# Kernel optimization log

Measured on AMD Instinct MI355X. Metric: run time of the kernel, lower is better.

The kernel has to match this reference:

```python
import jax, jax.numpy as jnp
import numpy as np

HEADS = 8


def setup_inputs() -> dict:
    key = jax.random.key(0)
    ks = jax.random.split(key, 4)
    b, n, dim, inner = 8, 1024, 512, 512
    x = jax.random.normal(ks[0], (b, n, dim), jnp.float32)
    cp_mask = jax.random.randint(ks[1], (n, n), 0, 2, jnp.int32)  # binary core-periphery mask
    w_qkv = jax.random.normal(ks[2], (dim, 3 * inner), jnp.float32) * 0.02
    w_out = jax.random.normal(ks[3], (inner, dim), jnp.float32) * 0.02
    b_out = jnp.zeros((dim,), jnp.float32)
    return {"x": x, "cp_mask": cp_mask, "w_qkv": w_qkv, "w_out": w_out,
            "b_out": b_out, "patches_in_core_nodes": 16}


def reference(x, cp_mask, w_qkv, w_out, b_out, patches_in_core_nodes):
    b, n, dim = x.shape
    inner = w_qkv.shape[1] // 3
    dh = inner // HEADS
    scale = dh ** -0.5

    qkv = x @ w_qkv                                   # [b, n, 3*inner]
    q, k, v = jnp.split(qkv, 3, axis=-1)
    split_heads = lambda t: t.reshape(b, n, HEADS, dh).transpose(0, 2, 1, 3)
    q, k, v = map(split_heads, (q, k, v))             # [b, h, n, dh]

    mask = cp_mask.astype(x.dtype)                    # [n, n]
    dots_raw = jnp.einsum('bhnd,bhmd->bhnm', q, k)    # [b, h, n, n]

    # analysis pass: per-row mean |masked score|, summed over heads (detached in original)
    nnz = jnp.count_nonzero(cp_mask, axis=1).astype(x.dtype)       # [n]
    score = (jnp.abs(dots_raw * mask) * scale).sum(axis=1).sum(axis=-1) / nnz  # [b, n]
    score = jax.lax.stop_gradient(score)
    # original: list(np.argsort(score)) then list.reverse() -> batch order reversed
    idx = jnp.argsort(score, axis=-1)[::-1]           # [b, n]

    attn = jax.nn.softmax(dots_raw * scale * mask, axis=-1)
    out = jnp.einsum('bhnm,bhmd->bhnd', attn, v)      # [b, h, n, dh]
    out = out.transpose(0, 2, 1, 3).reshape(b, n, inner)

    # sequential row swap: out[j,i] <-> out[j,idx[j,i]] using the pristine clone
    out_clone = out
    bi = jnp.arange(b)
    for i in range(1, patches_in_core_nodes + 1):
        ti = idx[:, i]                                # [b]
        out = out.at[bi, i].set(out_clone[bi, ti])
        out = out.at[bi, ti].set(out_clone[:, i])
    return out @ w_out + b_out
```

## Files before the change

kernel.cpp:

```cpp
#include <hip/hip_runtime.h>
#include <hip/hip_bf16.h>

#define NN 1024
#define DH 64
#define DIM 512
#define INNER 512
#define QKV_N 1536
#define SCALE 0.125f
#define KPITCH 72
#define VPITCH 68
#define GPITCH 40

typedef short short8 __attribute__((ext_vector_type(8)));
typedef short short4v __attribute__((ext_vector_type(4)));
typedef float floatx4 __attribute__((ext_vector_type(4)));

static __device__ __forceinline__ unsigned short f2bf(float x) {
  __hip_bfloat16 h = __float2bfloat16(x);
  unsigned short u;
  __builtin_memcpy(&u, &h, 2);
  return u;
}
static __device__ __forceinline__ void splitbf(float x, unsigned short& hi, unsigned short& lo) {
  __hip_bfloat16 h = __float2bfloat16(x);
  float hf = __bfloat162float(h);
  __hip_bfloat16 l = __float2bfloat16(x - hf);
  __builtin_memcpy(&hi, &h, 2);
  __builtin_memcpy(&lo, &l, 2);
}

__global__ __launch_bounds__(64) void nnz_kernel(const int* __restrict__ mask,
                                                 float* __restrict__ nnzf,
                                                 unsigned long long* __restrict__ Mbits) {
  int row = blockIdx.x;
  int lane = threadIdx.x;
  const int* mrow = mask + (size_t)row * NN;
  int tot = 0;
  for (int mt = 0; mt < 16; ++mt) {
    unsigned long long bits = __ballot(mrow[mt * 64 + lane] != 0);
    if (lane == 0) {
      Mbits[(size_t)row * 16 + mt] = bits;
      tot += __popcll(bits);
    }
  }
  if (lane == 0) nnzf[row] = (float)tot;
}

__global__ __launch_bounds__(256) void split_kernel(const float* __restrict__ in,
                                                    unsigned short* __restrict__ hi,
                                                    unsigned short* __restrict__ lo,
                                                    int n4) {
  int i = blockIdx.x * 256 + threadIdx.x;
  if (i >= n4) return;
  float4 v = ((const float4*)in)[i];
  ushort4 h, l;
  splitbf(v.x, h.x, l.x);
  splitbf(v.y, h.y, l.y);
  splitbf(v.z, h.z, l.z);
  splitbf(v.w, h.w, l.w);
  ((ushort4*)hi)[i] = h;
  ((ushort4*)lo)[i] = l;
}

__global__ __launch_bounds__(256) void tsplit_kernel(const float* __restrict__ in, int K, int N,
                                                     unsigned short* __restrict__ hiT,
                                                     unsigned short* __restrict__ loT) {
  __shared__ float tile[32][33];
  int n0 = blockIdx.x * 32, k0 = blockIdx.y * 32;
  int t = threadIdx.x;
  int tn = t & 31, tk = t >> 5;
#pragma unroll
  for (int i = 0; i < 32; i += 8)
    tile[tk + i][tn] = in[(size_t)(k0 + tk + i) * N + n0 + tn];
  __syncthreads();
#pragma unroll
  for (int i = 0; i < 32; i += 8) {
    int n = tk + i;
    float v = tile[tn][n];
    unsigned short h, l;
    splitbf(v, h, l);
    hiT[(size_t)(n0 + n) * K + k0 + tn] = h;
    loT[(size_t)(n0 + n) * K + k0 + tn] = l;
  }
}

__global__ __launch_bounds__(256) void qkv_mfma(const unsigned short* __restrict__ xhi,
                                                const unsigned short* __restrict__ xlo,
                                                const unsigned short* __restrict__ bhiT,
                                                const unsigned short* __restrict__ bloT,
                                                unsigned short* __restrict__ qhi,
                                                unsigned short* __restrict__ qlo,
                                                unsigned short* __restrict__ khi,
                                                unsigned short* __restrict__ klo,
                                                unsigned short* __restrict__ vb) {
  __shared__ __align__(16) unsigned short Ah[128][GPITCH], Al[128][GPITCH];
  __shared__ __align__(16) unsigned short Bh[128][GPITCH], Bl[128][GPITCH];
  int t = threadIdx.x;
  int lane = t & 63, w = t >> 6;
  int wr = w >> 1, wc = w & 1;
  int s = lane & 15, q4 = lane >> 4;
  int r0 = blockIdx.y * 128, c0 = blockIdx.x * 128;

  floatx4 acc[4][4];
#pragma unroll
  for (int mi = 0; mi < 4; ++mi)
#pragma unroll
    for (int ni = 0; ni < 4; ++ni) { acc[mi][ni][0] = 0.f; acc[mi][ni][1] = 0.f; acc[mi][ni][2] = 0.f; acc[mi][ni][3] = 0.f; }

  for (int kt = 0; kt < DIM; kt += 32) {
    __syncthreads();
#pragma unroll
    for (int p = 0; p < 2; ++p) {
      int idx = p * 256 + t;
      int row = idx >> 2, kc = (idx & 3) * 8;
      *(short8*)&Ah[row][kc] = *(const short8*)&xhi[(size_t)(r0 + row) * DIM + kt + kc];
      *(short8*)&Al[row][kc] = *(const short8*)&xlo[(size_t)(r0 + row) * DIM + kt + kc];
      *(short8*)&Bh[row][kc] = *(const short8*)&bhiT[(size_t)(c0 + row) * DIM + kt + kc];
      *(short8*)&Bl[row][kc] = *(const short8*)&bloT[(size_t)(c0 + row) * DIM + kt + kc];
    }
    __syncthreads();
    short8 ah[4], al[4], bhf[4], blf[4];
#pragma unroll
    for (int mi = 0; mi < 4; ++mi) {
      ah[mi] = *(const short8*)&Ah[wr * 64 + mi * 16 + s][q4 * 8];
      al[mi] = *(const short8*)&Al[wr * 64 + mi * 16 + s][q4 * 8];
    }
#pragma unroll
    for (int ni = 0; ni < 4; ++ni) {
      bhf[ni] = *(const short8*)&Bh[wc * 64 + ni * 16 + s][q4 * 8];
      blf[ni] = *(const short8*)&Bl[wc * 64 + ni * 16 + s][q4 * 8];
    }
#pragma unroll
    for (int mi = 0; mi < 4; ++mi)
#pragma unroll
      for (int ni = 0; ni < 4; ++ni) {
        acc[mi][ni] = __builtin_amdgcn_mfma_f32_16x16x32_bf16(al[mi], bhf[ni], acc[mi][ni], 0, 0, 0);
        acc[mi][ni] = __builtin_amdgcn_mfma_f32_16x16x32_bf16(ah[mi], blf[ni], acc[mi][ni], 0, 0, 0);
        acc[mi][ni] = __builtin_amdgcn_mfma_f32_16x16x32_bf16(ah[mi], bhf[ni], acc[mi][ni], 0, 0, 0);
      }
  }

  int which = c0 >> 9;
#pragma unroll
  for (int mi = 0; mi < 4; ++mi)
#pragma unroll
    for (int ni = 0; ni < 4; ++ni) {
      int Cl = c0 + wc * 64 + ni * 16 + s;
      int cc = Cl & 511, h = cc >> 6, d = cc & 63;
#pragma unroll
      for (int i = 0; i < 4; ++i) {
        int R = r0 + wr * 64 + mi * 16 + q4 * 4 + i;
        int b = R >> 10, n = R & 1023;
        size_t o = (size_t)((((b << 3) + h) << 10) + n) * DH + d;
        float v = acc[mi][ni][i];
        if (which == 0) {
          unsigned short hh, ll;
          splitbf(SCALE * v, hh, ll);
          qhi[o] = hh; qlo[o] = ll;
        } else if (which == 1) {
          unsigned short hh, ll;
          splitbf(v, hh, ll);
          khi[o] = hh; klo[o] = ll;
        } else {
          vb[o] = f2bf(v);
        }
      }
    }
}

__global__ __launch_bounds__(256, 4) void attn_kernel(const unsigned short* __restrict__ qhi,
                                                      const unsigned short* __restrict__ qlo,
                                                      const unsigned short* __restrict__ khi,
                                                      const unsigned short* __restrict__ klo,
                                                      const unsigned short* __restrict__ vb,
                                                      const unsigned long long* __restrict__ Mbits,
                                                      unsigned short* __restrict__ ohi,
                                                      unsigned short* __restrict__ olo,
                                                      float* __restrict__ sph) {
  int bh = blockIdx.y;
  int rb = blockIdx.x;
  int b = bh >> 3, h = bh & 7;
  int row0 = rb * 64;
  int t = threadIdx.x;
  int lane = t & 63, w = t >> 6;
  int q4 = lane >> 4, s = lane & 15;
  int gr = 16 * w + s;

  __shared__ __align__(16) unsigned short Khs[64][KPITCH], Kls[64][KPITCH];
  __shared__ __align__(16) unsigned short Vts[64][VPITCH];
  __shared__ __align__(16) unsigned short Pss[64][KPITCH];
  __shared__ unsigned long long Mb[64];

  short8 aqh[2], aql[2];
  {
    size_t qb0 = ((size_t)bh * NN + row0 + gr) * DH;
#pragma unroll
    for (int ks = 0; ks < 2; ++ks) {
      aqh[ks] = *(const short8*)&qhi[qb0 + ks * 32 + q4 * 8];
      aql[ks] = *(const short8*)&qlo[qb0 + ks * 32 + q4 * 8];
    }
  }

  floatx4 Oacc[4];
  float Lacc[4], Sco[4];
#pragma unroll
  for (int j = 0; j < 4; ++j) { Oacc[j][0] = 0.f; Oacc[j][1] = 0.f; Oacc[j][2] = 0.f; Oacc[j][3] = 0.f; }
#pragma unroll
  for (int i = 0; i < 4; ++i) { Lacc[i] = 0.f; Sco[i] = 0.f; }

  for (int mt = 0; mt < 16; ++mt) {
    int m0 = mt * 64;
    __syncthreads();
#pragma unroll
    for (int p = 0; p < 2; ++p) {
      int idx = p * 256 + t;
      int n = idx >> 3, c8 = (idx & 7) * 8;
      size_t g = ((size_t)bh * NN + m0 + n) * DH + c8;
      *(short8*)&Khs[n][c8] = *(const short8*)&khi[g];
      *(short8*)&Kls[n][c8] = *(const short8*)&klo[g];
      short8 vv = *(const short8*)&vb[g];
#pragma unroll
      for (int j = 0; j < 8; ++j) Vts[c8 + j][n] = (unsigned short)vv[j];
    }
    if (t < 64) Mb[t] = Mbits[(size_t)(row0 + t) * 16 + mt];
    __syncthreads();

    floatx4 Sf[4];
#pragma unroll
    for (int j = 0; j < 4; ++j) { Sf[j][0] = 0.f; Sf[j][1] = 0.f; Sf[j][2] = 0.f; Sf[j][3] = 0.f; }
#pragma unroll
    for (int ks = 0; ks < 2; ++ks) {
      int d0 = ks * 32 + q4 * 8;
#pragma unroll
      for (int j = 0; j < 4; ++j) {
        short8 kh8 = *(const short8*)&Khs[16 * j + s][d0];
        short8 kl8 = *(const short8*)&Kls[16 * j + s][d0];
        Sf[j] = __builtin_amdgcn_mfma_f32_16x16x32_bf16(aql[ks], kh8, Sf[j], 0, 0, 0);
        Sf[j] = __builtin_amdgcn_mfma_f32_16x16x32_bf16(aqh[ks], kl8, Sf[j], 0, 0, 0);
        Sf[j] = __builtin_amdgcn_mfma_f32_16x16x32_bf16(aqh[ks], kh8, Sf[j], 0, 0, 0);
      }
    }

    unsigned long long mb[4];
#pragma unroll
    for (int i = 0; i < 4; ++i) mb[i] = Mb[16 * w + 4 * q4 + i];
    unsigned short pw[4][4];
#pragma unroll
    for (int j = 0; j < 4; ++j) {
#pragma unroll
      for (int i = 0; i < 4; ++i) {
        float sv = Sf[j][i];
        float mf = ((mb[i] >> (16 * j + s)) & 1ULL) ? 1.0f : 0.0f;
        Sco[i] += fabsf(sv) * mf;
        float p = __expf(sv * mf);
        Lacc[i] += p;
        pw[i][j] = f2bf(p);
      }
    }

#pragma unroll
    for (int i = 0; i < 4; ++i)
#pragma unroll
      for (int j = 0; j < 4; ++j) Pss[16 * w + 4 * q4 + i][16 * j + s] = pw[i][j];

#pragma unroll
    for (int ks = 0; ks < 2; ++ks) {
      int mm0 = ks * 32 + q4 * 8;
      short8 ap = *(const short8*)&Pss[gr][mm0];
#pragma unroll
      for (int j = 0; j < 4; ++j) {
        short8 bv;
        *(short4v*)&bv = *(const short4v*)&Vts[16 * j + s][mm0];
        *(((short4v*)&bv) + 1) = *(const short4v*)&Vts[16 * j + s][mm0 + 4];
        Oacc[j] = __builtin_amdgcn_mfma_f32_16x16x32_bf16(ap, bv, Oacc[j], 0, 0, 0);
      }
    }
  }

#pragma unroll
  for (int off = 1; off < 16; off <<= 1) {
#pragma unroll
    for (int i = 0; i < 4; ++i) {
      Lacc[i] += __shfl_xor(Lacc[i], off, 16);
      Sco[i] += __shfl_xor(Sco[i], off, 16);
    }
  }
#pragma unroll
  for (int i = 0; i < 4; ++i) {
    int r = row0 + 16 * w + 4 * q4 + i;
    float iv = 1.0f / Lacc[i];
#pragma unroll
    for (int j = 0; j < 4; ++j) {
      float o = Oacc[j][i] * iv;
      unsigned short hh, ll;
      splitbf(o, hh, ll);
      size_t oo = (size_t)((b << 10) + r) * INNER + (h << 6) + 16 * j + s;
      ohi[oo] = hh; olo[oo] = ll;
    }
    if (s == 0) sph[((size_t)bh << 10) + r] = Sco[i];
  }
}

__global__ __launch_bounds__(256) void score_reduce(const float* __restrict__ sph,
                                                    const float* __restrict__ nnzf,
                                                    float* __restrict__ score) {
  int g = blockIdx.x * 256 + threadIdx.x;
  int b = g >> 10, r = g & 1023;
  float sv = 0.f;
#pragma unroll
  for (int h = 0; h < 8; ++h) sv += sph[(size_t)(((b << 3) + h) << 10) + r];
  score[g] = sv / nnzf[r];
}

__global__ __launch_bounds__(256) void select_kernel(const float* __restrict__ score,
                                                     const int* __restrict__ pic_ptr,
                                                     int* __restrict__ asc) {
  int bb = blockIdx.x;
  int t = threadIdx.x;
  int cnt = pic_ptr[0] + 1;
  __shared__ float sv[1024];
  __shared__ float rv[256];
  __shared__ int ri[256];
  for (int i = t; i < 1024; i += 256) sv[i] = score[(size_t)bb * 1024 + i];
  __syncthreads();
  for (int sel = 0; sel < cnt; ++sel) {
    float bv = 3.4e38f; int bi = 1 << 30;
    for (int i = t; i < 1024; i += 256) {
      float v = sv[i];
      if (v < bv) { bv = v; bi = i; }
    }
    rv[t] = bv; ri[t] = bi;
    __syncthreads();
    for (int s2 = 128; s2 > 0; s2 >>= 1) {
      if (t < s2) {
        float ov = rv[t + s2]; int oi = ri[t + s2];
        if (ov < rv[t] || (ov == rv[t] && oi < ri[t])) { rv[t] = ov; ri[t] = oi; }
      }
      __syncthreads();
    }
    if (t == 0) {
      asc[bb * 32 + sel] = ri[0];
      sv[ri[0]] = 3.4e38f;
    }
    __syncthreads();
  }
}

__global__ __launch_bounds__(256) void build_src(const int* __restrict__ asc,
                                                 const int* __restrict__ pic_ptr,
                                                 int* __restrict__ src) {
  int bi = blockIdx.x;
  int t = threadIdx.x;
  for (int r = t; r < 1024; r += 256) src[bi * 1024 + r] = r;
  __syncthreads();
  if (t == 0) {
    int pic = pic_ptr[0];
    const int* a = &asc[(7 - bi) * 32];
    for (int i = 1; i <= pic; ++i) {
      int ti = a[i];
      src[bi * 1024 + i] = ti;
      src[bi * 1024 + ti] = i;
    }
  }
}

__global__ __launch_bounds__(256) void out_mfma(const unsigned short* __restrict__ ahi,
                                                const unsigned short* __restrict__ alo,
                                                const unsigned short* __restrict__ bhiT,
                                                const unsigned short* __restrict__ bloT,
                                                const float* __restrict__ bias,
                                                const int* __restrict__ src,
                                                float* __restrict__ C) {
  __shared__ __align__(16) unsigned short Ah[128][GPITCH], Al[128][GPITCH];
  __shared__ __align__(16) unsigned short Bh[128][GPITCH], Bl[128][GPITCH];
  int t = threadIdx.x;
  int lane = t & 63, w = t >> 6;
  int wr = w >> 1, wc = w & 1;
  int s = lane & 15, q4 = lane >> 4;
  int r0 = blockIdx.y * 128, c0 = blockIdx.x * 128;
  int bb = r0 >> 10;

  int grow[2];
#pragma unroll
  for (int p = 0; p < 2; ++p) {
    int idx = p * 256 + t;
    grow[p] = (bb << 10) + src[r0 + (idx >> 2)];
  }

  floatx4 acc[4][4];
#pragma unroll
  for (int mi = 0; mi < 4; ++mi)
#pragma unroll
    for (int ni = 0; ni < 4; ++ni) { acc[mi][ni][0] = 0.f; acc[mi][ni][1] = 0.f; acc[mi][ni][2] = 0.f; acc[mi][ni][3] = 0.f; }

  for (int kt = 0; kt < INNER; kt += 32) {
    __syncthreads();
#pragma unroll
    for (int p = 0; p < 2; ++p) {
      int idx = p * 256 + t;
      int row = idx >> 2, kc = (idx & 3) * 8;
      *(short8*)&Ah[row][kc] = *(const short8*)&ahi[(size_t)grow[p] * INNER + kt + kc];
      *(short8*)&Al[row][kc] = *(const short8*)&alo[(size_t)grow[p] * INNER + kt + kc];
      *(short8*)&Bh[row][kc] = *(const short8*)&bhiT[(size_t)(c0 + row) * INNER + kt + kc];
      *(short8*)&Bl[row][kc] = *(const short8*)&bloT[(size_t)(c0 + row) * INNER + kt + kc];
    }
    __syncthreads();
    short8 ah[4], al[4], bhf[4], blf[4];
#pragma unroll
    for (int mi = 0; mi < 4; ++mi) {
      ah[mi] = *(const short8*)&Ah[wr * 64 + mi * 16 + s][q4 * 8];
      al[mi] = *(const short8*)&Al[wr * 64 + mi * 16 + s][q4 * 8];
    }
#pragma unroll
    for (int ni = 0; ni < 4; ++ni) {
      bhf[ni] = *(const short8*)&Bh[wc * 64 + ni * 16 + s][q4 * 8];
      blf[ni] = *(const short8*)&Bl[wc * 64 + ni * 16 + s][q4 * 8];
    }
#pragma unroll
    for (int mi = 0; mi < 4; ++mi)
#pragma unroll
      for (int ni = 0; ni < 4; ++ni) {
        acc[mi][ni] = __builtin_amdgcn_mfma_f32_16x16x32_bf16(al[mi], bhf[ni], acc[mi][ni], 0, 0, 0);
        acc[mi][ni] = __builtin_amdgcn_mfma_f32_16x16x32_bf16(ah[mi], blf[ni], acc[mi][ni], 0, 0, 0);
        acc[mi][ni] = __builtin_amdgcn_mfma_f32_16x16x32_bf16(ah[mi], bhf[ni], acc[mi][ni], 0, 0, 0);
      }
  }

#pragma unroll
  for (int ni = 0; ni < 4; ++ni) {
    int Cl = c0 + wc * 64 + ni * 16 + s;
    float bv = bias[Cl];
#pragma unroll
    for (int mi = 0; mi < 4; ++mi)
#pragma unroll
      for (int i = 0; i < 4; ++i) {
        int R = r0 + wr * 64 + mi * 16 + q4 * 4 + i;
        C[(size_t)R * DIM + Cl] = acc[mi][ni][i] + bv;
      }
  }
}

extern "C" void kernel_launch(void* const* d_in, const int* in_sizes, int n_in,
                              void* d_out, int out_size, void* d_ws, size_t ws_size,
                              hipStream_t stream) {
  const float* x      = (const float*)d_in[0];
  const int*   cpmask = (const int*)d_in[1];
  const float* w_qkv  = (const float*)d_in[2];
  const float* w_out  = (const float*)d_in[3];
  const float* b_out  = (const float*)d_in[4];
  const int*   pic    = (const int*)d_in[5];
  float* out = (float*)d_out;

  unsigned short* xhi   = (unsigned short*)d_ws;
  unsigned short* xlo   = xhi + 4194304;
  unsigned short* wqhiT = xlo + 4194304;
  unsigned short* wqloT = wqhiT + 786432;
  unsigned short* wohiT = wqloT + 786432;
  unsigned short* woloT = wohiT + 262144;
  unsigned short* qhi   = woloT + 262144;
  unsigned short* qlo   = qhi + 4194304;
  unsigned short* khi   = qlo + 4194304;
  unsigned short* klo   = khi + 4194304;
  unsigned short* vbp   = klo + 4194304;
  float* sph  = (float*)(vbp + 4194304);
  float* sc   = sph + 65536;
  float* nnzf = sc + 8192;
  int*   asc  = (int*)(nnzf + 1024);
  int*   src  = asc + 512;
  unsigned long long* Mbits = (unsigned long long*)(src + 8192);

  unsigned short* ohi = xhi;
  unsigned short* olo = xlo;

  hipLaunchKernelGGL(nnz_kernel,   dim3(1024),    dim3(64),  0, stream, cpmask, nnzf, Mbits);
  hipLaunchKernelGGL(split_kernel, dim3(4096),    dim3(256), 0, stream, x, xhi, xlo, 1048576);
  hipLaunchKernelGGL(tsplit_kernel, dim3(48, 16), dim3(256), 0, stream, w_qkv, DIM, QKV_N, wqhiT, wqloT);
  hipLaunchKernelGGL(tsplit_kernel, dim3(16, 16), dim3(256), 0, stream, w_out, INNER, DIM, wohiT, woloT);
  hipLaunchKernelGGL(qkv_mfma,     dim3(12, 64),  dim3(256), 0, stream, xhi, xlo, wqhiT, wqloT,
                     qhi, qlo, khi, klo, vbp);
  hipLaunchKernelGGL(attn_kernel,  dim3(16, 64),  dim3(256), 0, stream, qhi, qlo, khi, klo, vbp,
                     Mbits, ohi, olo, sph);
  hipLaunchKernelGGL(score_reduce, dim3(32),      dim3(256), 0, stream, sph, nnzf, sc);
  hipLaunchKernelGGL(select_kernel, dim3(8),      dim3(256), 0, stream, sc, pic, asc);
  hipLaunchKernelGGL(build_src,    dim3(8),       dim3(256), 0, stream, asc, pic, src);
  hipLaunchKernelGGL(out_mfma,     dim3(4, 64),   dim3(256), 0, stream, ohi, olo, wohiT, woloT,
                     b_out, src, out);
}
```

Measured before the change: 270.5 us.

## Use direct global-to-LDS loads, pre-transpose V, fuse score reduce and select

The GEMM tile loads in qkv_mfma and out_mfma now use global_load_lds with an unpadded LDS layout, so data skips the VGPR round trip. A separate vtrans kernel pre-transposes V, which lets the attention kernel load V tiles with vector stores instead of scattered transposing LDS writes. The attention block index is remapped so blocks that run together are spread across heads and batches. The score reduction is fused into the top-k selection kernel, which now reduces with wave shuffles instead of a shared-memory tree. The risks are bank conflicts from the unpadded LDS tiles, plus an extra kernel launch and extra traffic for V.

```diff
diff --git a/kernel.cpp b/kernel.cpp
--- a/kernel.cpp
+++ b/kernel.cpp
@@ -8,11 +8,8 @@
 #define QKV_N 1536
 #define SCALE 0.125f
 #define KPITCH 72
-#define VPITCH 68
-#define GPITCH 40
 
 typedef short short8 __attribute__((ext_vector_type(8)));
-typedef short short4v __attribute__((ext_vector_type(4)));
 typedef float floatx4 __attribute__((ext_vector_type(4)));
 
 static __device__ __forceinline__ unsigned short f2bf(float x) {
@@ -27,6 +24,11 @@
   __hip_bfloat16 l = __float2bfloat16(x - hf);
   __builtin_memcpy(&hi, &h, 2);
   __builtin_memcpy(&lo, &l, 2);
+}
+static __device__ __forceinline__ void gll16(const unsigned short* g, unsigned short* l) {
+  __builtin_amdgcn_global_load_lds(
+      (const __attribute__((address_space(1))) unsigned int*)g,
+      (__attribute__((address_space(3))) unsigned int*)l, 16, 0, 0);
 }
 
 __global__ __launch_bounds__(64) void nnz_kernel(const int* __restrict__ mask,
@@ -93,13 +95,15 @@
                                                 unsigned short* __restrict__ khi,
                                                 unsigned short* __restrict__ klo,
                                                 unsigned short* __restrict__ vb) {
-  __shared__ __align__(16) unsigned short Ah[128][GPITCH], Al[128][GPITCH];
-  __shared__ __align__(16) unsigned short Bh[128][GPITCH], Bl[128][GPITCH];
+  __shared__ __align__(16) unsigned short Ah[128 * 32], Al[128 * 32];
+  __shared__ __align__(16) unsigned short Bh[128 * 32], Bl[128 * 32];
   int t = threadIdx.x;
   int lane = t & 63, w = t >> 6;
   int wr = w >> 1, wc = w & 1;
   int s = lane & 15, q4 = lane >> 4;
   int r0 = blockIdx.y * 128, c0 = blockIdx.x * 128;
+  int kcol = (lane & 3) * 8;
+  int rA = lane >> 2;
 
   floatx4 acc[4][4];
 #pragma unroll
@@ -110,25 +114,26 @@
   for (int kt = 0; kt < DIM; kt += 32) {
     __syncthreads();
 #pragma unroll
-    for (int p = 0; p < 2; ++p) {
-      int idx = p * 256 + t;
-      int row = idx >> 2, kc = (idx & 3) * 8;
-      *(short8*)&Ah[row][kc] = *(const short8*)&xhi[(size_t)(r0 + row) * DIM + kt + kc];
-      *(short8*)&Al[row][kc] = *(const short8*)&xlo[(size_t)(r0 + row) * DIM + kt + kc];
-      *(short8*)&Bh[row][kc] = *(const short8*)&bhiT[(size_t)(c0 + row) * DIM + kt + kc];
-      *(short8*)&Bl[row][kc] = *(const short8*)&bloT[(size_t)(c0 + row) * DIM + kt + kc];
+    for (int c = 0; c < 2; ++c) {
+      int chunk = w * 2 + c;
+      int row = chunk * 16 + rA;
+      int lo_off = chunk * 512;
+      gll16(&xhi[(size_t)(r0 + row) * DIM + kt + kcol], &Ah[lo_off]);
+      gll16(&xlo[(size_t)(r0 + row) * DIM + kt + kcol], &Al[lo_off]);
+      gll16(&bhiT[(size_t)(c0 + row) * DIM + kt + kcol], &Bh[lo_off]);
+      gll16(&bloT[(size_t)(c0 + row) * DIM + kt + kcol], &Bl[lo_off]);
     }
     __syncthreads();
     short8 ah[4], al[4], bhf[4], blf[4];
 #pragma unroll
     for (int mi = 0; mi < 4; ++mi) {
-      ah[mi] = *(const short8*)&Ah[wr * 64 + mi * 16 + s][q4 * 8];
-      al[mi] = *(const short8*)&Al[wr * 64 + mi * 16 + s][q4 * 8];
+      ah[mi] = *(const short8*)&Ah[(wr * 64 + mi * 16 + s) * 32 + q4 * 8];
+      al[mi] = *(const short8*)&Al[(wr * 64 + mi * 16 + s) * 32 + q4 * 8];
     }
 #pragma unroll
     for (int ni = 0; ni < 4; ++ni) {
-      bhf[ni] = *(const short8*)&Bh[wc * 64 + ni * 16 + s][q4 * 8];
-      blf[ni] = *(const short8*)&Bl[wc * 64 + ni * 16 + s][q4 * 8];
+      bhf[ni] = *(const short8*)&Bh[(wc * 64 + ni * 16 + s) * 32 + q4 * 8];
+      blf[ni] = *(const short8*)&Bl[(wc * 64 + ni * 16 + s) * 32 + q4 * 8];
     }
 #pragma unroll
     for (int mi = 0; mi < 4; ++mi)
@@ -168,17 +173,45 @@
     }
 }
 
+__global__ __launch_bounds__(256) void vtrans(const unsigned short* __restrict__ vb,
+                                              unsigned short* __restrict__ vT) {
+  int bh = blockIdx.y, nt = blockIdx.x;
+  __shared__ __align__(16) unsigned short T[64][KPITCH];
+  int t = threadIdx.x;
+  {
+    int n = t >> 2, d0 = (t & 3) * 16;
+    const unsigned short* src = &vb[((size_t)bh * NN + nt * 64 + n) * DH + d0];
+    *(short8*)&T[n][d0] = *(const short8*)&src[0];
+    *(short8*)&T[n][d0 + 8] = *(const short8*)&src[8];
+  }
+  __syncthreads();
+  {
+    int d = t >> 2, n0 = (t & 3) * 16;
+    short8 o0, o1;
+#pragma unroll
+    for (int j = 0; j < 8; ++j) {
+      o0[j] = (short)T[n0 + j][d];
+      o1[j] = (short)T[n0 + 8 + j][d];
+    }
+    unsigned short* dst = &vT[((size_t)bh * DH + d) * NN + nt * 64 + n0];
+    *(short8*)&dst[0] = o0;
+    *(short8*)&dst[8] = o1;
+  }
+}
+
 __global__ __launch_bounds__(256, 4) void attn_kernel(const unsigned short* __restrict__ qhi,
                                                       const unsigned short* __restrict__ qlo,
                                                       const unsigned short* __restrict__ khi,
                                                       const unsigned short* __restrict__ klo,
-                                                      const unsigned short* __restrict__ vb,
+                                                      const unsigned short* __restrict__ vT,
                                                       const unsigned long long* __restrict__ Mbits,
                                                       unsigned short* __restrict__ ohi,
                                                       unsigned short* __restrict__ olo,
                                                       float* __restrict__ sph) {
-  int bh = blockIdx.y;
-  int rb = blockIdx.x;
+  int l = blockIdx.y * 16 + blockIdx.x;
+  int k = l >> 3;
+  int rb = k & 15;
+  int bh = (l & 7) + 8 * (k >> 4);
   int b = bh >> 3, h = bh & 7;
   int row0 = rb * 64;
   int t = threadIdx.x;
@@ -187,7 +220,7 @@
   int gr = 16 * w + s;
 
   __shared__ __align__(16) unsigned short Khs[64][KPITCH], Kls[64][KPITCH];
-  __shared__ __align__(16) unsigned short Vts[64][VPITCH];
+  __shared__ __align__(16) unsigned short Vts[64][KPITCH];
   __shared__ __align__(16) unsigned short Pss[64][KPITCH];
   __shared__ unsigned long long Mb[64];
 
@@ -218,9 +251,7 @@
       size_t g = ((size_t)bh * NN + m0 + n) * DH + c8;
       *(short8*)&Khs[n][c8] = *(const short8*)&khi[g];
       *(short8*)&Kls[n][c8] = *(const short8*)&klo[g];
-      short8 vv = *(const short8*)&vb[g];
-#pragma unroll
-      for (int j = 0; j < 8; ++j) Vts[c8 + j][n] = (unsigned short)vv[j];
+      *(short8*)&Vts[n][c8] = *(const short8*)&vT[((size_t)bh * DH + n) * NN + m0 + c8];
     }
     if (t < 64) Mb[t] = Mbits[(size_t)(row0 + t) * 16 + mt];
     __syncthreads();
@@ -269,9 +300,7 @@
       short8 ap = *(const short8*)&Pss[gr][mm0];
 #pragma unroll
       for (int j = 0; j < 4; ++j) {
-        short8 bv;
-        *(short4v*)&bv = *(const short4v*)&Vts[16 * j + s][mm0];
-        *(((short4v*)&bv) + 1) = *(const short4v*)&Vts[16 * j + s][mm0 + 4];
+        short8 bv = *(const short8*)&Vts[16 * j + s][mm0];
         Oacc[j] = __builtin_amdgcn_mfma_f32_16x16x32_bf16(ap, bv, Oacc[j], 0, 0, 0);
       }
     }
@@ -301,47 +330,52 @@
   }
 }
 
-__global__ __launch_bounds__(256) void score_reduce(const float* __restrict__ sph,
+__global__ __launch_bounds__(256) void score_select(const float* __restrict__ sph,
                                                     const float* __restrict__ nnzf,
-                                                    float* __restrict__ score) {
-  int g = blockIdx.x * 256 + threadIdx.x;
-  int b = g >> 10, r = g & 1023;
-  float sv = 0.f;
-#pragma unroll
-  for (int h = 0; h < 8; ++h) sv += sph[(size_t)(((b << 3) + h) << 10) + r];
-  score[g] = sv / nnzf[r];
-}
-
-__global__ __launch_bounds__(256) void select_kernel(const float* __restrict__ score,
-                                                     const int* __restrict__ pic_ptr,
-                                                     int* __restrict__ asc) {
+                                                    const int* __restrict__ pic_ptr,
+                                                    int* __restrict__ asc) {
   int bb = blockIdx.x;
   int t = threadIdx.x;
   int cnt = pic_ptr[0] + 1;
-  __shared__ float sv[1024];
-  __shared__ float rv[256];
-  __shared__ int ri[256];
-  for (int i = t; i < 1024; i += 256) sv[i] = score[(size_t)bb * 1024 + i];
-  __syncthreads();
+  float v[4];
+#pragma unroll
+  for (int i = 0; i < 4; ++i) {
+    int r = t + 256 * i;
+    float sv = 0.f;
+#pragma unroll
+    for (int h = 0; h < 8; ++h) sv += sph[(size_t)(((bb << 3) + h) << 10) + r];
+    v[i] = sv / nnzf[r];
+  }
+  __shared__ float wv[4];
+  __shared__ int wi[4];
+  __shared__ int bsel;
   for (int sel = 0; sel < cnt; ++sel) {
-    float bv = 3.4e38f; int bi = 1 << 30;
-    for (int i = t; i < 1024; i += 256) {
-      float v = sv[i];
-      if (v < bv) { bv = v; bi = i; }
-    }
-    rv[t] = bv; ri[t] = bi;
-    __syncthreads();
-    for (int s2 = 128; s2 > 0; s2 >>= 1) {
-      if (t < s2) {
-        float ov = rv[t + s2]; int oi = ri[t + s2];
-        if (ov < rv[t] || (ov == rv[t] && oi < ri[t])) { rv[t] = ov; ri[t] = oi; }
-      }
-      __syncthreads();
-    }
+    float bv = v[0];
+    int bi = t;
+#pragma unroll
+    for (int i = 1; i < 4; ++i) {
+      if (v[i] < bv) { bv = v[i]; bi = t + 256 * i; }
+    }
+#pragma unroll
+    for (int off = 1; off < 64; off <<= 1) {
+      float ov = __shfl_xor(bv, off, 64);
+      int oi = __shfl_xor(bi, off, 64);
+      if (ov < bv || (ov == bv && oi < bi)) { bv = ov; bi = oi; }
+    }
+    if ((t & 63) == 0) { wv[t >> 6] = bv; wi[t >> 6] = bi; }
+    __syncthreads();
     if (t == 0) {
-      asc[bb * 32 + sel] = ri[0];
-      sv[ri[0]] = 3.4e38f;
-    }
+      float B = wv[0]; int I = wi[0];
+#pragma unroll
+      for (int q = 1; q < 4; ++q) {
+        if (wv[q] < B || (wv[q] == B && wi[q] < I)) { B = wv[q]; I = wi[q]; }
+      }
+      bsel = I;
+      asc[bb * 32 + sel] = I;
+    }
+    __syncthreads();
+    int wloc = bsel - t;
+    if (wloc >= 0 && (wloc & 255) == 0 && wloc < 1024) v[wloc >> 8] = 3.4e38f;
     __syncthreads();
   }
 }
@@ -371,20 +405,22 @@
                                                 const float* __restrict__ bias,
                                                 const int* __restrict__ src,
                                                 float* __restrict__ C) {
-  __shared__ __align__(16) unsigned short Ah[128][GPITCH], Al[128][GPITCH];
-  __shared__ __align__(16) unsigned short Bh[128][GPITCH], Bl[128][GPITCH];
+  __shared__ __align__(16) unsigned short Ah[128 * 32], Al[128 * 32];
+  __shared__ __align__(16) unsigned short Bh[128 * 32], Bl[128 * 32];
   int t = threadIdx.x;
   int lane = t & 63, w = t >> 6;
   int wr = w >> 1, wc = w & 1;
   int s = lane & 15, q4 = lane >> 4;
   int r0 = blockIdx.y * 128, c0 = blockIdx.x * 128;
   int bb = r0 >> 10;
+  int kcol = (lane & 3) * 8;
+  int rA = lane >> 2;
 
   int grow[2];
 #pragma unroll
-  for (int p = 0; p < 2; ++p) {
-    int idx = p * 256 + t;
-    grow[p] = (bb << 10) + src[r0 + (idx >> 2)];
+  for (int c = 0; c < 2; ++c) {
+    int row = (w * 2 + c) * 16 + rA;
+    grow[c] = (bb << 10) + src[r0 + row];
   }
 
   floatx4 acc[4][4];
@@ -396,25 +432,26 @@
   for (int kt = 0; kt < INNER; kt += 32) {
     __syncthreads();
 #pragma unroll
-    for (int p = 0; p < 2; ++p) {
-      int idx = p * 256 + t;
-      int row = idx >> 2, kc = (idx & 3) * 8;
-      *(short8*)&Ah[row][kc] = *(const short8*)&ahi[(size_t)grow[p] * INNER + kt + kc];
-      *(short8*)&Al[row][kc] = *(const short8*)&alo[(size_t)grow[p] * INNER + kt + kc];
-      *(short8*)&Bh[row][kc] = *(const short8*)&bhiT[(size_t)(c0 + row) * INNER + kt + kc];
-      *(short8*)&Bl[row][kc] = *(const short8*)&bloT[(size_t)(c0 + row) * INNER + kt + kc];
+    for (int c = 0; c < 2; ++c) {
+      int chunk = w * 2 + c;
+      int row = chunk * 16 + rA;
+      int lo_off = chunk * 512;
+      gll16(&ahi[(size_t)grow[c] * INNER + kt + kcol], &Ah[lo_off]);
+      gll16(&alo[(size_t)grow[c] * INNER + kt + kcol], &Al[lo_off]);
+      gll16(&bhiT[(size_t)(c0 + row) * INNER + kt + kcol], &Bh[lo_off]);
+      gll16(&bloT[(size_t)(c0 + row) * INNER + kt + kcol], &Bl[lo_off]);
     }
     __syncthreads();
     short8 ah[4], al[4], bhf[4], blf[4];
 #pragma unroll
     for (int mi = 0; mi < 4; ++mi) {
-      ah[mi] = *(const short8*)&Ah[wr * 64 + mi * 16 + s][q4 * 8];
-      al[mi] = *(const short8*)&Al[wr * 64 + mi * 16 + s][q4 * 8];
+      ah[mi] = *(const short8*)&Ah[(wr * 64 + mi * 16 + s) * 32 + q4 * 8];
+      al[mi] = *(const short8*)&Al[(wr * 64 + mi * 16 + s) * 32 + q4 * 8];
     }
 #pragma unroll
     for (int ni = 0; ni < 4; ++ni) {
-      bhf[ni] = *(const short8*)&Bh[wc * 64 + ni * 16 + s][q4 * 8];
-      blf[ni] = *(const short8*)&Bl[wc * 64 + ni * 16 + s][q4 * 8];
+      bhf[ni] = *(const short8*)&Bh[(wc * 64 + ni * 16 + s) * 32 + q4 * 8];
+      blf[ni] = *(const short8*)&Bl[(wc * 64 + ni * 16 + s) * 32 + q4 * 8];
     }
 #pragma unroll
     for (int mi = 0; mi < 4; ++mi)
@@ -468,21 +505,22 @@
   int*   asc  = (int*)(nnzf + 1024);
   int*   src  = asc + 512;
   unsigned long long* Mbits = (unsigned long long*)(src + 8192);
+  unsigned short* vTp = (unsigned short*)(Mbits + 16384);
 
   unsigned short* ohi = xhi;
   unsigned short* olo = xlo;
 
-  hipLaunchKernelGGL(nnz_kernel,   dim3(1024),    dim3(64),  0, stream, cpmask, nnzf, Mbits);
-  hipLaunchKernelGGL(split_kernel, dim3(4096),    dim3(256), 0, stream, x, xhi, xlo, 1048576);
-  hipLaunchKernelGGL(tsplit_kernel, dim3(48, 16), dim3(256), 0, stream, w_qkv, DIM, QKV_N, wqhiT, wqloT);
-  hipLaunchKernelGGL(tsplit_kernel, dim3(16, 16), dim3(256), 0, stream, w_out, INNER, DIM, wohiT, woloT);
-  hipLaunchKernelGGL(qkv_mfma,     dim3(12, 64),  dim3(256), 0, stream, xhi, xlo, wqhiT, wqloT,
+  hipLaunchKernelGGL(nnz_kernel,    dim3(1024),    dim3(64),  0, stream, cpmask, nnzf, Mbits);
+  hipLaunchKernelGGL(split_kernel,  dim3(4096),    dim3(256), 0, stream, x, xhi, xlo, 1048576);
+  hipLaunchKernelGGL(tsplit_kernel, dim3(48, 16),  dim3(256), 0, stream, w_qkv, DIM, QKV_N, wqhiT, wqloT);
+  hipLaunchKernelGGL(tsplit_kernel, dim3(16, 16),  dim3(256), 0, stream, w_out, INNER, DIM, wohiT, woloT);
+  hipLaunchKernelGGL(qkv_mfma,      dim3(12, 64),  dim3(256), 0, stream, xhi, xlo, wqhiT, wqloT,
                      qhi, qlo, khi, klo, vbp);
-  hipLaunchKernelGGL(attn_kernel,  dim3(16, 64),  dim3(256), 0, stream, qhi, qlo, khi, klo, vbp,
+  hipLaunchKernelGGL(vtrans,        dim3(16, 64),  dim3(256), 0, stream, vbp, vTp);
+  hipLaunchKernelGGL(attn_kernel,   dim3(16, 64),  dim3(256), 0, stream, qhi, qlo, khi, klo, vTp,
                      Mbits, ohi, olo, sph);
-  hipLaunchKernelGGL(score_reduce, dim3(32),      dim3(256), 0, stream, sph, nnzf, sc);
-  hipLaunchKernelGGL(select_kernel, dim3(8),      dim3(256), 0, stream, sc, pic, asc);
-  hipLaunchKernelGGL(build_src,    dim3(8),       dim3(256), 0, stream, asc, pic, src);
-  hipLaunchKernelGGL(out_mfma,     dim3(4, 64),   dim3(256), 0, stream, ohi, olo, wohiT, woloT,
+  hipLaunchKernelGGL(score_select,  dim3(8),       dim3(256), 0, stream, sph, nnzf, pic, asc);
+  hipLaunchKernelGGL(build_src,     dim3(8),       dim3(256), 0, stream, asc, pic, src);
+  hipLaunchKernelGGL(out_mfma,      dim3(4, 64),   dim3(256), 0, stream, ohi, olo, wohiT, woloT,
                      b_out, src, out);
 }
```

Measured after the change: 258.6 us. 1.05x faster.
